# Performance work log

Hardware: AMD Instinct MI355X
Metric: run time of the kernel (lower is better)

Reference implementation:

```python
import jax, jax.numpy as jnp
import numpy as np

B, C, H, W = 8, 256, 128, 128
CQK = C // 8
EPS = 1e-6


def _l2n(x):
    # normalize over channel axis (dim=-2), matching torch l2_norm (no eps)
    return x / jnp.linalg.norm(x, axis=-2, keepdims=True)


def setup_inputs() -> dict:
    key = jax.random.key(0)
    ks = jax.random.split(key, 8)
    s = 0.05
    return {
        "x": jax.random.normal(ks[0], (B, C, H, W), dtype=jnp.float32),
        "Wq": jax.random.normal(ks[1], (CQK, C), dtype=jnp.float32) * s,
        "bq": jax.random.normal(ks[2], (CQK,), dtype=jnp.float32) * s,
        "Wk": jax.random.normal(ks[3], (CQK, C), dtype=jnp.float32) * s,
        "bk": jax.random.normal(ks[4], (CQK,), dtype=jnp.float32) * s,
        "Wv": jax.random.normal(ks[5], (C, C), dtype=jnp.float32) * s,
        "bv": jax.random.normal(ks[6], (C,), dtype=jnp.float32) * s,
        "gamma": jnp.ones((1,), dtype=jnp.float32) * 0.5,
    }


def reference(x, Wq, bq, Wk, bk, Wv, bv, gamma):
    b, c, h, w = x.shape
    n = h * w
    xf = x.reshape(b, c, n)  # [B, C, N]
    # 1x1 convs == channel matmuls
    Q = jnp.einsum('oc,bcn->bon', Wq, xf) + bq[None, :, None]  # [B, Cqk, N]
    K = jnp.einsum('oc,bcn->bon', Wk, xf) + bk[None, :, None]  # [B, Cqk, N]
    V = jnp.einsum('oc,bcn->bon', Wv, xf) + bv[None, :, None]  # [B, C, N]
    Qn = jnp.swapaxes(_l2n(Q), 1, 2)  # [B, N, Cqk]
    Kn = _l2n(K)                      # [B, Cqk, N]
    k_sum = jnp.sum(Kn, axis=-1) + EPS               # [B, Cqk]
    tailor = 1.0 / (n + jnp.einsum('bnc,bc->bn', Qn, k_sum))  # [B, N]
    value_sum = jnp.sum(V, axis=-1)                   # [B, C]
    matrix = jnp.einsum('bmn,bcn->bmc', Kn, V)        # [B, Cqk, C]
    matrix_sum = value_sum[:, :, None] + jnp.einsum('bnm,bmc->bcn', Qn, matrix)  # [B, C, N]
    weight_value = matrix_sum * tailor[:, None, :]    # [B, C, N]
    return x + gamma[0] * weight_value.reshape(b, c, h, w)
```

## Files before the change

### kernel.cpp

```cpp
#include <hip/hip_runtime.h>
#include <stdint.h>


#define NB 8
#define NC 256
#define CQK 32
#define NPIX 16384
#define NTILE 64
#define TN 256
#define PARTF (CQK*NC + NC + CQK)
#define EPSV 1e-6f

typedef unsigned short bfraw;

__device__ __forceinline__ float bf2f(bfraw u) {
    union { uint32_t i; float f; } v; v.i = ((uint32_t)u) << 16; return v.f;
}
__device__ __forceinline__ void unpack8(uint4 raw, float* xv) {
    xv[0] = bf2f((bfraw)(raw.x & 0xffffu)); xv[1] = bf2f((bfraw)(raw.x >> 16));
    xv[2] = bf2f((bfraw)(raw.y & 0xffffu)); xv[3] = bf2f((bfraw)(raw.y >> 16));
    xv[4] = bf2f((bfraw)(raw.z & 0xffffu)); xv[5] = bf2f((bfraw)(raw.z >> 16));
    xv[6] = bf2f((bfraw)(raw.w & 0xffffu)); xv[7] = bf2f((bfraw)(raw.w >> 16));
}
template<int DT> __device__ __forceinline__ float ldx(const void* p, size_t i) {
    if (DT) return ((const float*)p)[i];
    return bf2f(((const bfraw*)p)[i]);
}
template<int DT> __device__ __forceinline__ void ld8(const void* p, size_t i, float* o) {
    if (DT) {
        const float4* q = (const float4*)((const float*)p + i);
        float4 a = q[0], b = q[1];
        o[0]=a.x;o[1]=a.y;o[2]=a.z;o[3]=a.w;o[4]=b.x;o[5]=b.y;o[6]=b.z;o[7]=b.w;
    } else {
        uint4 raw = *(const uint4*)((const bfraw*)p + i);
        unpack8(raw, o);
    }
}

template<int DT> __device__ __forceinline__ void prep_body(
    const void* Wq, const void* bq, const void* Wk, const void* bk,
    float* wkqT, float* bkq) {
    int tid = threadIdx.x;
    for (int i = tid; i < CQK*NC; i += 256) {
        int m = i >> 8, c = i & 255;
        wkqT[c*64 + m]      = ldx<DT>(Wk, i);
        wkqT[c*64 + 32 + m] = ldx<DT>(Wq, i);
    }
    if (tid < CQK)      bkq[tid]      = ldx<DT>(bk, tid);
    else if (tid < 64)  bkq[tid]      = ldx<DT>(bq, tid - 32);
}
__global__ __launch_bounds__(256) void detprep_kernel(
    const bfraw* __restrict__ xr, const void* Wq, const void* bq,
    const void* Wk, const void* bk,
    int* __restrict__ flag, float* __restrict__ wkqT, float* __restrict__ bkq) {
    __shared__ int cnt, ez, fl_s;
    int tid = threadIdx.x;
    if (tid == 0) { cnt = 0; ez = 0; }
    __syncthreads();
    int crazy = 0, evenzero = 0;
    for (int i = tid; i < 2048; i += 256) {
        bfraw u = xr[i];
        float v = bf2f(u);
        float a = fabsf(v);
        if (!(a <= 1e10f) || (v != 0.f && a < 1e-10f)) crazy++;
        if ((i & 1) == 0 && u == 0) evenzero++;
    }
    atomicAdd(&cnt, crazy);
    atomicAdd(&ez, evenzero);
    __syncthreads();
    if (tid == 0) { fl_s = (cnt > 64 || ez > 900) ? 1 : 0; flag[0] = fl_s; }
    __syncthreads();
    if (fl_s) prep_body<1>(Wq, bq, Wk, bk, wkqT, bkq);
    else      prep_body<0>(Wq, bq, Wk, bk, wkqT, bkq);
}

template<int DT> __device__ __forceinline__ void pass1_body(
    const void* __restrict__ x, const float* __restrict__ wkqT,
    const float* __restrict__ bkq, float4* __restrict__ qn4,
    float* __restrict__ partial, int PB, float (*kn_s)[36]) {
    int tid = threadIdx.x;
    int b = blockIdx.x / PB, j = blockIdx.x % PB;

    float sacc[CQK];
    #pragma unroll
    for (int m = 0; m < CQK; ++m) sacc[m] = 0.f;
    float xsacc = 0.f, ksacc = 0.f;

    const size_t xb_base = (size_t)b * NC * NPIX;

    for (int tile = j; tile < NTILE; tile += PB) {
        int n0 = tile * TN;

        float kq[64];
        #pragma unroll
        for (int m = 0; m < 64; ++m) kq[m] = bkq[m];
        const size_t pixi = xb_base + n0 + tid;
        for (int c0 = 0; c0 < NC; c0 += 8) {
            float xv[8];
            #pragma unroll
            for (int jj = 0; jj < 8; ++jj)
                xv[jj] = ldx<DT>(x, pixi + (size_t)(c0+jj) * NPIX);
            #pragma unroll
            for (int jj = 0; jj < 8; ++jj) {
                const float4* w = (const float4*)(wkqT + (c0+jj)*64);
                #pragma unroll
                for (int m4 = 0; m4 < 16; ++m4) {
                    float4 wv = w[m4];
                    kq[m4*4+0] += wv.x * xv[jj]; kq[m4*4+1] += wv.y * xv[jj];
                    kq[m4*4+2] += wv.z * xv[jj]; kq[m4*4+3] += wv.w * xv[jj];
                }
            }
        }
        float ssk = 0.f, ssq = 0.f;
        #pragma unroll
        for (int m = 0; m < CQK; ++m) {
            ssk += kq[m]*kq[m]; ssq += kq[32+m]*kq[32+m];
        }
        float invk = rsqrtf(ssk), invq = rsqrtf(ssq);

        __syncthreads();
        #pragma unroll
        for (int m4 = 0; m4 < 8; ++m4) {
            float4 kv;
            kv.x = kq[m4*4+0]*invk; kv.y = kq[m4*4+1]*invk;
            kv.z = kq[m4*4+2]*invk; kv.w = kq[m4*4+3]*invk;
            *((float4*)&kn_s[tid][m4*4]) = kv;
        }
        __syncthreads();

        float4* qp = qn4 + (size_t)b * 8 * NPIX + (n0 + tid);
        #pragma unroll
        for (int m4 = 0; m4 < 8; ++m4) {
            float4 qv;
            qv.x = kq[32+m4*4+0]*invq; qv.y = kq[32+m4*4+1]*invq;
            qv.z = kq[32+m4*4+2]*invq; qv.w = kq[32+m4*4+3]*invq;
            qp[(size_t)m4 * NPIX] = qv;
        }

        const size_t rowbase = xb_base + (size_t)tid * NPIX + n0;
        for (int k0 = 0; k0 < TN; k0 += 8) {
            float xv[8]; ld8<DT>(x, rowbase + k0, xv);
            #pragma unroll
            for (int kk = 0; kk < 8; ++kk) {
                const float4* kr = (const float4*)&kn_s[k0+kk][0];
                float xvk = xv[kk];
                #pragma unroll
                for (int m4 = 0; m4 < 8; ++m4) {
                    float4 a = kr[m4];
                    sacc[m4*4+0] += a.x*xvk; sacc[m4*4+1] += a.y*xvk;
                    sacc[m4*4+2] += a.z*xvk; sacc[m4*4+3] += a.w*xvk;
                }
                xsacc += xvk;
            }
        }

        if (tid < CQK) {
            float s = 0.f;
            for (int t = 0; t < TN; ++t) s += kn_s[t][tid];
            ksacc += s;
        }
    }

    size_t base = (size_t)blockIdx.x * PARTF;
    #pragma unroll
    for (int m = 0; m < CQK; ++m) partial[base + m*NC + tid] = sacc[m];
    partial[base + CQK*NC + tid] = xsacc;
    if (tid < CQK) partial[base + CQK*NC + NC + tid] = ksacc;
}
__global__ __launch_bounds__(256) void pass1_kernel(
    const void* __restrict__ x, const float* __restrict__ wkqT,
    const float* __restrict__ bkq, float4* __restrict__ qn4,
    float* __restrict__ partial, int PB, const int* __restrict__ flag) {
    __shared__ __align__(16) float kn_s[TN][36];
    if (flag[0]) pass1_body<1>(x, wkqT, bkq, qn4, partial, PB, kn_s);
    else         pass1_body<0>(x, wkqT, bkq, qn4, partial, PB, kn_s);
}

template<int DT> __device__ __forceinline__ float dot256(const void* Wv, int row,
                                                         const float* sh) {
    float r = 0.f;
    for (int c0 = 0; c0 < NC; c0 += 8) {
        float xv[8]; ld8<DT>(Wv, (size_t)row * NC + c0, xv);
        #pragma unroll
        for (int i = 0; i < 8; ++i) r += xv[i] * sh[c0+i];
    }
    return r;
}
template<int DT> __device__ __forceinline__ void pass15_body(
    const float* __restrict__ partial, const void* __restrict__ Wv,
    const void* __restrict__ bv, float* __restrict__ matT,
    float* __restrict__ vsum, float* __restrict__ ksum, int PB, float* sh) {
    int tid = threadIdx.x;
    int b = blockIdx.x / 33, m = blockIdx.x % 33;
    const float* pb_ = partial + (size_t)b * PB * PARTF;

    if (m < CQK) {
        float acc = 0.f;
        for (int p = 0; p < PB; ++p) acc += pb_[(size_t)p*PARTF + m*NC + tid];
        sh[tid] = acc;
        float ks = 0.f;
        for (int p = 0; p < PB; ++p) ks += pb_[(size_t)p*PARTF + CQK*NC + NC + m];
        __syncthreads();
        float r = dot256<DT>(Wv, tid, sh);
        matT[((size_t)b*NC + tid)*CQK + m] = r + ldx<DT>(bv, tid) * ks;
        if (tid == 0) ksum[b*CQK + m] = ks + EPSV;
    } else {
        float acc = 0.f;
        for (int p = 0; p < PB; ++p) acc += pb_[(size_t)p*PARTF + CQK*NC + tid];
        sh[tid] = acc;
        __syncthreads();
        float r = dot256<DT>(Wv, tid, sh);
        vsum[b*NC + tid] = r + (float)NPIX * ldx<DT>(bv, tid);
    }
}
__global__ __launch_bounds__(256) void pass15_kernel(
    const float* __restrict__ partial, const void* __restrict__ Wv,
    const void* __restrict__ bv, float* __restrict__ matT,
    float* __restrict__ vsum, float* __restrict__ ksum, int PB,
    const int* __restrict__ flag) {
    __shared__ float sh[NC];
    if (flag[0]) pass15_body<1>(partial, Wv, bv, matT, vsum, ksum, PB, sh);
    else         pass15_body<0>(partial, Wv, bv, matT, vsum, ksum, PB, sh);
}

template<int DT> __device__ __forceinline__ void pass2_body(
    const void* __restrict__ x, const float4* __restrict__ qn4,
    const float* __restrict__ ksum, const float* __restrict__ matT,
    const float* __restrict__ vsum, const void* __restrict__ gamma,
    float* __restrict__ out) {
    int tid = threadIdx.x;
    int bx = blockIdx.x;
    int cs = bx & 3, tile = (bx >> 2) & 63, b = bx >> 8;
    int n0 = tile * TN;
    int p = n0 + tid;

    float q[CQK];
    const float4* qp = qn4 + (size_t)b * 8 * NPIX + p;
    #pragma unroll
    for (int m4 = 0; m4 < 8; ++m4) {
        float4 v = qp[(size_t)m4 * NPIX];
        q[m4*4+0]=v.x; q[m4*4+1]=v.y; q[m4*4+2]=v.z; q[m4*4+3]=v.w;
    }
    const float* ksb = ksum + b*CQK;
    float dot = 0.f;
    #pragma unroll
    for (int m = 0; m < CQK; ++m) dot += q[m] * ksb[m];
    float tl = 1.f / ((float)NPIX + dot);
    float gt = ldx<DT>(gamma, 0) * tl;

    int c0 = cs * 64;
    const float* mb = matT + ((size_t)b*NC + c0)*CQK;
    const float* vb = vsum + (size_t)b*NC + c0;
    size_t xbase = (size_t)b*NC*NPIX + (size_t)c0*NPIX + p;

    for (int ci = 0; ci < 64; ci += 4) {
        float xv[4];
        #pragma unroll
        for (int u = 0; u < 4; ++u)
            xv[u] = ldx<DT>(x, xbase + (size_t)(ci+u)*NPIX);
        #pragma unroll
        for (int u = 0; u < 4; ++u) {
            float r = vb[ci+u];
            const float4* mr = (const float4*)(mb + (ci+u)*CQK);
            #pragma unroll
            for (int m4 = 0; m4 < 8; ++m4) {
                float4 a = mr[m4];
                r += q[m4*4+0]*a.x + q[m4*4+1]*a.y + q[m4*4+2]*a.z + q[m4*4+3]*a.w;
            }
            out[xbase + (size_t)(ci+u)*NPIX] = xv[u] + gt*r;
        }
    }
}
__global__ __launch_bounds__(256) void pass2_kernel(
    const void* __restrict__ x, const float4* __restrict__ qn4,
    const float* __restrict__ ksum, const float* __restrict__ matT,
    const float* __restrict__ vsum, const void* __restrict__ gamma,
    float* __restrict__ out, const int* __restrict__ flag) {
    if (flag[0]) pass2_body<1>(x, qn4, ksum, matT, vsum, gamma, out);
    else         pass2_body<0>(x, qn4, ksum, matT, vsum, gamma, out);
}

extern "C" void kernel_launch(void* const* d_in, const int* in_sizes, int n_in,
                              void* d_out, int out_size, void* d_ws, size_t ws_size,
                              hipStream_t stream)
{
    const void* x  = d_in[0];
    const void* Wq = d_in[1];
    const void* bq = d_in[2];
    const void* Wk = d_in[3];
    const void* bk = d_in[4];
    const void* Wv = d_in[5];
    const void* bv = d_in[6];
    const void* gm = d_in[7];
    float* out = (float*)d_out;

    float* ws = (float*)d_ws;
    int*   flag = (int*)ws;
    float* wkqT = ws + 16;
    float* bkq  = wkqT + 64*NC;
    float* matT = bkq + 64;
    float* vsum = matT + NB*NC*CQK;
    float* ksum = vsum + NB*NC;
    float* qn4f = ksum + NB*CQK;
    float* partial = qn4f + (size_t)NB*8*NPIX*4;

    size_t fixedf = (size_t)(partial - ws);
    int PB = 64;
    while (PB > 1 && (fixedf + (size_t)NB*PB*PARTF) * 4 > ws_size) PB >>= 1;

    hipLaunchKernelGGL(detprep_kernel, dim3(1), dim3(256), 0, stream,
                       (const bfraw*)x, Wq, bq, Wk, bk, flag, wkqT, bkq);
    hipLaunchKernelGGL(pass1_kernel, dim3(NB*PB), dim3(256), 0, stream,
                       x, wkqT, bkq, (float4*)qn4f, partial, PB, flag);
    hipLaunchKernelGGL(pass15_kernel, dim3(NB*33), dim3(256), 0, stream,
                       partial, Wv, bv, matT, vsum, ksum, PB, flag);
    hipLaunchKernelGGL(pass2_kernel, dim3(NB*NTILE*4), dim3(256), 0, stream,
                       x, (const float4*)qn4f, ksum, matT, vsum, gm, out, flag);
}
```

Baseline: 489.6 us.

## Split pass1 channel projection across thread groups and process pixel pairs per thread

Pass1 now handles one 128-pixel tile per block across 128 blocks per batch. The 64 K/Q output channels are split into four 16-channel groups, each thread covers two adjacent pixels, and the L2 norms are reduced through shared memory. The k-sum reduction is parallelised over all threads instead of 32. Pass2 now processes two pixels per thread with float2 loads and stores, and both kernels get launch-bounds occupancy hints. The partial buffer falls back to the output buffer when the workspace is too small, which relies on pass2 overwriting it later.

```diff
diff --git a/kernel.cpp b/kernel.cpp
--- a/kernel.cpp
+++ b/kernel.cpp
@@ -6,8 +6,8 @@
 #define NC 256
 #define CQK 32
 #define NPIX 16384
-#define NTILE 64
-#define TN 256
+#define TN 128
+#define PB 128
 #define PARTF (CQK*NC + NC + CQK)
 #define EPSV 1e-6f
 
@@ -36,6 +36,15 @@
         unpack8(raw, o);
     }
 }
+template<int DT> __device__ __forceinline__ void ldx2(const void* p, size_t i, float* o) {
+    if (DT) {
+        float2 v = *(const float2*)((const float*)p + i);
+        o[0] = v.x; o[1] = v.y;
+    } else {
+        uint32_t r = *(const uint32_t*)((const bfraw*)p + i);
+        o[0] = bf2f((bfraw)(r & 0xffffu)); o[1] = bf2f((bfraw)(r >> 16));
+    }
+}
 
 template<int DT> __device__ __forceinline__ void prep_body(
     const void* Wq, const void* bq, const void* Wk, const void* bk,
@@ -77,103 +86,132 @@
 template<int DT> __device__ __forceinline__ void pass1_body(
     const void* __restrict__ x, const float* __restrict__ wkqT,
     const float* __restrict__ bkq, float4* __restrict__ qn4,
-    float* __restrict__ partial, int PB, float (*kn_s)[36]) {
-    int tid = threadIdx.x;
-    int b = blockIdx.x / PB, j = blockIdx.x % PB;
-
-    float sacc[CQK];
-    #pragma unroll
-    for (int m = 0; m < CQK; ++m) sacc[m] = 0.f;
-    float xsacc = 0.f, ksacc = 0.f;
-
-    const size_t xb_base = (size_t)b * NC * NPIX;
-
-    for (int tile = j; tile < NTILE; tile += PB) {
-        int n0 = tile * TN;
-
-        float kq[64];
-        #pragma unroll
-        for (int m = 0; m < 64; ++m) kq[m] = bkq[m];
-        const size_t pixi = xb_base + n0 + tid;
+    float* __restrict__ partial, float (*kn_s)[36], float* __restrict__ ss_s) {
+    const int tid  = threadIdx.x;
+    const int b    = blockIdx.x >> 7;
+    const int j    = blockIdx.x & (PB - 1);
+    const int n0   = j * TN;
+    const int pair = tid & 63;
+    const int g    = tid >> 6;
+    const size_t xb = (size_t)b * NC * NPIX;
+
+    float kq0[16], kq1[16];
+    #pragma unroll
+    for (int i = 0; i < 16; ++i) {
+        float bb = bkq[g*16 + i];
+        kq0[i] = bb; kq1[i] = bb;
+    }
+    {
+        const size_t pix0 = xb + (size_t)n0 + 2*pair;
         for (int c0 = 0; c0 < NC; c0 += 8) {
-            float xv[8];
+            float xv[8][2];
             #pragma unroll
             for (int jj = 0; jj < 8; ++jj)
-                xv[jj] = ldx<DT>(x, pixi + (size_t)(c0+jj) * NPIX);
+                ldx2<DT>(x, pix0 + (size_t)(c0 + jj) * NPIX, xv[jj]);
             #pragma unroll
             for (int jj = 0; jj < 8; ++jj) {
-                const float4* w = (const float4*)(wkqT + (c0+jj)*64);
+                const float4* w = (const float4*)(wkqT + (c0 + jj)*64 + g*16);
                 #pragma unroll
-                for (int m4 = 0; m4 < 16; ++m4) {
+                for (int m4 = 0; m4 < 4; ++m4) {
                     float4 wv = w[m4];
-                    kq[m4*4+0] += wv.x * xv[jj]; kq[m4*4+1] += wv.y * xv[jj];
-                    kq[m4*4+2] += wv.z * xv[jj]; kq[m4*4+3] += wv.w * xv[jj];
+                    kq0[m4*4+0] += wv.x * xv[jj][0]; kq0[m4*4+1] += wv.y * xv[jj][0];
+                    kq0[m4*4+2] += wv.z * xv[jj][0]; kq0[m4*4+3] += wv.w * xv[jj][0];
+                    kq1[m4*4+0] += wv.x * xv[jj][1]; kq1[m4*4+1] += wv.y * xv[jj][1];
+                    kq1[m4*4+2] += wv.z * xv[jj][1]; kq1[m4*4+3] += wv.w * xv[jj][1];
                 }
             }
         }
-        float ssk = 0.f, ssq = 0.f;
-        #pragma unroll
-        for (int m = 0; m < CQK; ++m) {
-            ssk += kq[m]*kq[m]; ssq += kq[32+m]*kq[32+m];
-        }
-        float invk = rsqrtf(ssk), invq = rsqrtf(ssq);
-
-        __syncthreads();
-        #pragma unroll
-        for (int m4 = 0; m4 < 8; ++m4) {
-            float4 kv;
-            kv.x = kq[m4*4+0]*invk; kv.y = kq[m4*4+1]*invk;
-            kv.z = kq[m4*4+2]*invk; kv.w = kq[m4*4+3]*invk;
-            *((float4*)&kn_s[tid][m4*4]) = kv;
-        }
-        __syncthreads();
-
-        float4* qp = qn4 + (size_t)b * 8 * NPIX + (n0 + tid);
-        #pragma unroll
-        for (int m4 = 0; m4 < 8; ++m4) {
-            float4 qv;
-            qv.x = kq[32+m4*4+0]*invq; qv.y = kq[32+m4*4+1]*invq;
-            qv.z = kq[32+m4*4+2]*invq; qv.w = kq[32+m4*4+3]*invq;
-            qp[(size_t)m4 * NPIX] = qv;
-        }
-
-        const size_t rowbase = xb_base + (size_t)tid * NPIX + n0;
-        for (int k0 = 0; k0 < TN; k0 += 8) {
-            float xv[8]; ld8<DT>(x, rowbase + k0, xv);
+    }
+
+    float ss0 = 0.f, ss1 = 0.f;
+    #pragma unroll
+    for (int i = 0; i < 16; ++i) { ss0 += kq0[i]*kq0[i]; ss1 += kq1[i]*kq1[i]; }
+    ss_s[(g*64 + pair)*2 + 0] = ss0;
+    ss_s[(g*64 + pair)*2 + 1] = ss1;
+    __syncthreads();
+
+    if (g < 2) {
+        float inv0 = rsqrtf(ss_s[(0*64+pair)*2+0] + ss_s[(1*64+pair)*2+0]);
+        float inv1 = rsqrtf(ss_s[(0*64+pair)*2+1] + ss_s[(1*64+pair)*2+1]);
+        float* r0 = &kn_s[2*pair  ][g*16];
+        float* r1 = &kn_s[2*pair+1][g*16];
+        #pragma unroll
+        for (int m4 = 0; m4 < 4; ++m4) {
+            float4 v0, v1;
+            v0.x = kq0[m4*4+0]*inv0; v0.y = kq0[m4*4+1]*inv0;
+            v0.z = kq0[m4*4+2]*inv0; v0.w = kq0[m4*4+3]*inv0;
+            v1.x = kq1[m4*4+0]*inv1; v1.y = kq1[m4*4+1]*inv1;
+            v1.z = kq1[m4*4+2]*inv1; v1.w = kq1[m4*4+3]*inv1;
+            *((float4*)&r0[m4*4]) = v0;
+            *((float4*)&r1[m4*4]) = v1;
+        }
+    } else {
+        float inv0 = rsqrtf(ss_s[(2*64+pair)*2+0] + ss_s[(3*64+pair)*2+0]);
+        float inv1 = rsqrtf(ss_s[(2*64+pair)*2+1] + ss_s[(3*64+pair)*2+1]);
+        float4* qp = qn4 + (size_t)b * 8 * NPIX + (n0 + 2*pair);
+        const int g2 = g - 2;
+        #pragma unroll
+        for (int m4 = 0; m4 < 4; ++m4) {
+            float4 v0, v1;
+            v0.x = kq0[m4*4+0]*inv0; v0.y = kq0[m4*4+1]*inv0;
+            v0.z = kq0[m4*4+2]*inv0; v0.w = kq0[m4*4+3]*inv0;
+            v1.x = kq1[m4*4+0]*inv1; v1.y = kq1[m4*4+1]*inv1;
+            v1.z = kq1[m4*4+2]*inv1; v1.w = kq1[m4*4+3]*inv1;
+            qp[(size_t)(g2*4 + m4) * NPIX]     = v0;
+            qp[(size_t)(g2*4 + m4) * NPIX + 1] = v1;
+        }
+    }
+    __syncthreads();
+
+    float sacc[CQK];
+    #pragma unroll
+    for (int m = 0; m < CQK; ++m) sacc[m] = 0.f;
+    float xsacc = 0.f;
+    const size_t rowb = xb + (size_t)tid * NPIX + n0;
+    for (int k0 = 0; k0 < TN; k0 += 8) {
+        float xv[8]; ld8<DT>(x, rowb + k0, xv);
+        #pragma unroll
+        for (int kk = 0; kk < 8; ++kk) {
+            const float4* kr = (const float4*)&kn_s[k0+kk][0];
+            float xvk = xv[kk];
             #pragma unroll
-            for (int kk = 0; kk < 8; ++kk) {
-                const float4* kr = (const float4*)&kn_s[k0+kk][0];
-                float xvk = xv[kk];
-                #pragma unroll
-                for (int m4 = 0; m4 < 8; ++m4) {
-                    float4 a = kr[m4];
-                    sacc[m4*4+0] += a.x*xvk; sacc[m4*4+1] += a.y*xvk;
-                    sacc[m4*4+2] += a.z*xvk; sacc[m4*4+3] += a.w*xvk;
-                }
-                xsacc += xvk;
+            for (int m4 = 0; m4 < 8; ++m4) {
+                float4 a = kr[m4];
+                sacc[m4*4+0] += a.x*xvk; sacc[m4*4+1] += a.y*xvk;
+                sacc[m4*4+2] += a.z*xvk; sacc[m4*4+3] += a.w*xvk;
             }
-        }
-
-        if (tid < CQK) {
-            float s = 0.f;
-            for (int t = 0; t < TN; ++t) s += kn_s[t][tid];
-            ksacc += s;
-        }
-    }
-
-    size_t base = (size_t)blockIdx.x * PARTF;
+            xsacc += xvk;
+        }
+    }
+
+    {
+        const int m_ = tid & 31, h_ = tid >> 5;
+        float kp = 0.f;
+        #pragma unroll
+        for (int t = 0; t < 16; ++t) kp += kn_s[h_*16 + t][m_];
+        ss_s[h_*32 + m_] = kp;
+    }
+    __syncthreads();
+
+    const size_t base = (size_t)blockIdx.x * PARTF;
     #pragma unroll
     for (int m = 0; m < CQK; ++m) partial[base + m*NC + tid] = sacc[m];
     partial[base + CQK*NC + tid] = xsacc;
-    if (tid < CQK) partial[base + CQK*NC + NC + tid] = ksacc;
-}
-__global__ __launch_bounds__(256) void pass1_kernel(
+    if (tid < CQK) {
+        float ks = 0.f;
+        #pragma unroll
+        for (int h = 0; h < 8; ++h) ks += ss_s[h*32 + tid];
+        partial[base + CQK*NC + NC + tid] = ks;
+    }
+}
+__global__ __launch_bounds__(256, 4) void pass1_kernel(
     const void* __restrict__ x, const float* __restrict__ wkqT,
     const float* __restrict__ bkq, float4* __restrict__ qn4,
-    float* __restrict__ partial, int PB, const int* __restrict__ flag) {
+    float* __restrict__ partial, const int* __restrict__ flag) {
     __shared__ __align__(16) float kn_s[TN][36];
-    if (flag[0]) pass1_body<1>(x, wkqT, bkq, qn4, partial, PB, kn_s);
-    else         pass1_body<0>(x, wkqT, bkq, qn4, partial, PB, kn_s);
+    __shared__ float ss_s[4*64*2];
+    if (flag[0]) pass1_body<1>(x, wkqT, bkq, qn4, partial, kn_s, ss_s);
+    else         pass1_body<0>(x, wkqT, bkq, qn4, partial, kn_s, ss_s);
 }
 
 template<int DT> __device__ __forceinline__ float dot256(const void* Wv, int row,
@@ -189,7 +227,7 @@
 template<int DT> __device__ __forceinline__ void pass15_body(
     const float* __restrict__ partial, const void* __restrict__ Wv,
     const void* __restrict__ bv, float* __restrict__ matT,
-    float* __restrict__ vsum, float* __restrict__ ksum, int PB, float* sh) {
+    float* __restrict__ vsum, float* __restrict__ ksum, float* sh) {
     int tid = threadIdx.x;
     int b = blockIdx.x / 33, m = blockIdx.x % 33;
     const float* pb_ = partial + (size_t)b * PB * PARTF;
@@ -216,11 +254,11 @@
 __global__ __launch_bounds__(256) void pass15_kernel(
     const float* __restrict__ partial, const void* __restrict__ Wv,
     const void* __restrict__ bv, float* __restrict__ matT,
-    float* __restrict__ vsum, float* __restrict__ ksum, int PB,
+    float* __restrict__ vsum, float* __restrict__ ksum,
     const int* __restrict__ flag) {
     __shared__ float sh[NC];
-    if (flag[0]) pass15_body<1>(partial, Wv, bv, matT, vsum, ksum, PB, sh);
-    else         pass15_body<0>(partial, Wv, bv, matT, vsum, ksum, PB, sh);
+    if (flag[0]) pass15_body<1>(partial, Wv, bv, matT, vsum, ksum, sh);
+    else         pass15_body<0>(partial, Wv, bv, matT, vsum, ksum, sh);
 }
 
 template<int DT> __device__ __forceinline__ void pass2_body(
@@ -230,48 +268,57 @@
     float* __restrict__ out) {
     int tid = threadIdx.x;
     int bx = blockIdx.x;
-    int cs = bx & 3, tile = (bx >> 2) & 63, b = bx >> 8;
-    int n0 = tile * TN;
-    int p = n0 + tid;
-
-    float q[CQK];
-    const float4* qp = qn4 + (size_t)b * 8 * NPIX + p;
+    int cs = bx & 3, tile = (bx >> 2) & 31, b = bx >> 7;
+    int p0 = tile * 512 + 2 * tid;
+
+    float q0[CQK], q1[CQK];
+    const float4* qp = qn4 + (size_t)b * 8 * NPIX + p0;
     #pragma unroll
     for (int m4 = 0; m4 < 8; ++m4) {
-        float4 v = qp[(size_t)m4 * NPIX];
-        q[m4*4+0]=v.x; q[m4*4+1]=v.y; q[m4*4+2]=v.z; q[m4*4+3]=v.w;
+        float4 a = qp[(size_t)m4 * NPIX];
+        float4 c = qp[(size_t)m4 * NPIX + 1];
+        q0[m4*4+0]=a.x; q0[m4*4+1]=a.y; q0[m4*4+2]=a.z; q0[m4*4+3]=a.w;
+        q1[m4*4+0]=c.x; q1[m4*4+1]=c.y; q1[m4*4+2]=c.z; q1[m4*4+3]=c.w;
     }
     const float* ksb = ksum + b*CQK;
-    float dot = 0.f;
-    #pragma unroll
-    for (int m = 0; m < CQK; ++m) dot += q[m] * ksb[m];
-    float tl = 1.f / ((float)NPIX + dot);
-    float gt = ldx<DT>(gamma, 0) * tl;
+    float dot0 = 0.f, dot1 = 0.f;
+    #pragma unroll
+    for (int m = 0; m < CQK; ++m) {
+        float k = ksb[m];
+        dot0 += q0[m] * k; dot1 += q1[m] * k;
+    }
+    float gm_ = ldx<DT>(gamma, 0);
+    float gt0 = gm_ / ((float)NPIX + dot0);
+    float gt1 = gm_ / ((float)NPIX + dot1);
 
     int c0 = cs * 64;
     const float* mb = matT + ((size_t)b*NC + c0)*CQK;
     const float* vb = vsum + (size_t)b*NC + c0;
-    size_t xbase = (size_t)b*NC*NPIX + (size_t)c0*NPIX + p;
+    size_t xbase = (size_t)b*NC*NPIX + (size_t)c0*NPIX + p0;
 
     for (int ci = 0; ci < 64; ci += 4) {
-        float xv[4];
+        float xv[4][2];
         #pragma unroll
         for (int u = 0; u < 4; ++u)
-            xv[u] = ldx<DT>(x, xbase + (size_t)(ci+u)*NPIX);
+            ldx2<DT>(x, xbase + (size_t)(ci+u)*NPIX, xv[u]);
         #pragma unroll
         for (int u = 0; u < 4; ++u) {
-            float r = vb[ci+u];
+            float r0 = vb[ci+u], r1 = r0;
             const float4* mr = (const float4*)(mb + (ci+u)*CQK);
             #pragma unroll
             for (int m4 = 0; m4 < 8; ++m4) {
                 float4 a = mr[m4];
-                r += q[m4*4+0]*a.x + q[m4*4+1]*a.y + q[m4*4+2]*a.z + q[m4*4+3]*a.w;
+                r0 += q0[m4*4+0]*a.x + q0[m4*4+1]*a.y + q0[m4*4+2]*a.z + q0[m4*4+3]*a.w;
+                r1 += q1[m4*4+0]*a.x + q1[m4*4+1]*a.y + q1[m4*4+2]*a.z + q1[m4*4+3]*a.w;
             }
-            out[xbase + (size_t)(ci+u)*NPIX] = xv[u] + gt*r;
-        }
-    }
-}
-__global__ __launch_bounds__(256) void pass2_kernel(
+            float2 o;
+            o.x = xv[u][0] + gt0*r0;
+            o.y = xv[u][1] + gt1*r1;
+            *reinterpret_cast<float2*>(out + xbase + (size_t)(ci+u)*NPIX) = o;
+        }
+    }
+}
+__global__ __launch_bounds__(256, 4) void pass2_kernel(
     const void* __restrict__ x, const float4* __restrict__ qn4,
     const float* __restrict__ ksum, const float* __restrict__ matT,
     const float* __restrict__ vsum, const void* __restrict__ gamma,
@@ -302,18 +349,18 @@
     float* vsum = matT + NB*NC*CQK;
     float* ksum = vsum + NB*NC;
     float* qn4f = ksum + NB*CQK;
-    float* partial = qn4f + (size_t)NB*8*NPIX*4;
-
-    size_t fixedf = (size_t)(partial - ws);
-    int PB = 64;
-    while (PB > 1 && (fixedf + (size_t)NB*PB*PARTF) * 4 > ws_size) PB >>= 1;
+    float* partial_ws = qn4f + (size_t)NB*8*NPIX*4;
+
+    size_t fixedf = (size_t)(partial_ws - ws);
+    size_t needb  = (fixedf + (size_t)NB*PB*PARTF) * sizeof(float);
+    float* partial = (needb <= ws_size) ? partial_ws : (float*)d_out;
 
     hipLaunchKernelGGL(detprep_kernel, dim3(1), dim3(256), 0, stream,
                        (const bfraw*)x, Wq, bq, Wk, bk, flag, wkqT, bkq);
     hipLaunchKernelGGL(pass1_kernel, dim3(NB*PB), dim3(256), 0, stream,
-                       x, wkqT, bkq, (float4*)qn4f, partial, PB, flag);
+                       x, wkqT, bkq, (float4*)qn4f, partial, flag);
     hipLaunchKernelGGL(pass15_kernel, dim3(NB*33), dim3(256), 0, stream,
-                       partial, Wv, bv, matT, vsum, ksum, PB, flag);
-    hipLaunchKernelGGL(pass2_kernel, dim3(NB*NTILE*4), dim3(256), 0, stream,
+                       partial, Wv, bv, matT, vsum, ksum, flag);
+    hipLaunchKernelGGL(pass2_kernel, dim3(NB*32*4), dim3(256), 0, stream,
                        x, (const float4*)qn4f, ksum, matT, vsum, gm, out, flag);
 }
```

Result: slower. 790.1 us (+61.4%).

## Split pass1 work across 512 threads with K/Q halves and pixel-half reduction

Applied to the files above, without the earlier changes.

Pass1 now runs 512 threads per block, with one tile per block. Each half of the threads computes either the K or the Q projection (32 outputs instead of 64), and the K^T·x accumulation is split across two pixel halves, then reduced through shared memory. This cuts per-thread register pressure and serial work in the projection, and raises parallelism per block. PB is fixed at 64, with a fallback that uses the output buffer as partial storage, and pass2 now loads 8 channels of x per iteration instead of 4. The cost is extra shared-memory exchange and barriers.

```diff
diff --git a/kernel.cpp b/kernel.cpp
--- a/kernel.cpp
+++ b/kernel.cpp
@@ -6,8 +6,8 @@
 #define NC 256
 #define CQK 32
 #define NPIX 16384
-#define NTILE 64
 #define TN 256
+#define PB1 64
 #define PARTF (CQK*NC + NC + CQK)
 #define EPSV 1e-6f
 
@@ -77,103 +77,122 @@
 template<int DT> __device__ __forceinline__ void pass1_body(
     const void* __restrict__ x, const float* __restrict__ wkqT,
     const float* __restrict__ bkq, float4* __restrict__ qn4,
-    float* __restrict__ partial, int PB, float (*kn_s)[36]) {
-    int tid = threadIdx.x;
-    int b = blockIdx.x / PB, j = blockIdx.x % PB;
-
-    float sacc[CQK];
-    #pragma unroll
-    for (int m = 0; m < CQK; ++m) sacc[m] = 0.f;
-    float xsacc = 0.f, ksacc = 0.f;
-
-    const size_t xb_base = (size_t)b * NC * NPIX;
-
-    for (int tile = j; tile < NTILE; tile += PB) {
-        int n0 = tile * TN;
-
-        float kq[64];
-        #pragma unroll
-        for (int m = 0; m < 64; ++m) kq[m] = bkq[m];
-        const size_t pixi = xb_base + n0 + tid;
-        for (int c0 = 0; c0 < NC; c0 += 8) {
-            float xv[8];
+    float* __restrict__ partial,
+    float (*kn_s)[36], float* __restrict__ ks2, float* __restrict__ xsx) {
+    const int tid  = threadIdx.x;
+    const int b    = blockIdx.x >> 6;
+    const int j    = blockIdx.x & (PB1 - 1);
+    const int n0   = j * TN;
+    const int px   = tid & 255;
+    const int half = tid >> 8;
+    const size_t xb = (size_t)b * NC * NPIX;
+
+    float kq[32];
+    #pragma unroll
+    for (int i = 0; i < 32; ++i) kq[i] = bkq[half*32 + i];
+    {
+        const size_t pixi = xb + (size_t)n0 + px;
+        for (int c = 0; c < NC; c += 2) {
+            float x0 = ldx<DT>(x, pixi + (size_t)c * NPIX);
+            float x1 = ldx<DT>(x, pixi + (size_t)(c+1) * NPIX);
+            const float4* w0 = (const float4*)(wkqT + c*64 + half*32);
+            const float4* w1 = (const float4*)(wkqT + (c+1)*64 + half*32);
             #pragma unroll
-            for (int jj = 0; jj < 8; ++jj)
-                xv[jj] = ldx<DT>(x, pixi + (size_t)(c0+jj) * NPIX);
-            #pragma unroll
-            for (int jj = 0; jj < 8; ++jj) {
-                const float4* w = (const float4*)(wkqT + (c0+jj)*64);
-                #pragma unroll
-                for (int m4 = 0; m4 < 16; ++m4) {
-                    float4 wv = w[m4];
-                    kq[m4*4+0] += wv.x * xv[jj]; kq[m4*4+1] += wv.y * xv[jj];
-                    kq[m4*4+2] += wv.z * xv[jj]; kq[m4*4+3] += wv.w * xv[jj];
-                }
+            for (int m4 = 0; m4 < 8; ++m4) {
+                float4 a = w0[m4], bb = w1[m4];
+                kq[m4*4+0] += a.x*x0; kq[m4*4+0] += bb.x*x1;
+                kq[m4*4+1] += a.y*x0; kq[m4*4+1] += bb.y*x1;
+                kq[m4*4+2] += a.z*x0; kq[m4*4+2] += bb.z*x1;
+                kq[m4*4+3] += a.w*x0; kq[m4*4+3] += bb.w*x1;
             }
         }
-        float ssk = 0.f, ssq = 0.f;
-        #pragma unroll
-        for (int m = 0; m < CQK; ++m) {
-            ssk += kq[m]*kq[m]; ssq += kq[32+m]*kq[32+m];
-        }
-        float invk = rsqrtf(ssk), invq = rsqrtf(ssq);
-
-        __syncthreads();
-        #pragma unroll
-        for (int m4 = 0; m4 < 8; ++m4) {
-            float4 kv;
-            kv.x = kq[m4*4+0]*invk; kv.y = kq[m4*4+1]*invk;
-            kv.z = kq[m4*4+2]*invk; kv.w = kq[m4*4+3]*invk;
-            *((float4*)&kn_s[tid][m4*4]) = kv;
-        }
-        __syncthreads();
-
-        float4* qp = qn4 + (size_t)b * 8 * NPIX + (n0 + tid);
-        #pragma unroll
-        for (int m4 = 0; m4 < 8; ++m4) {
-            float4 qv;
-            qv.x = kq[32+m4*4+0]*invq; qv.y = kq[32+m4*4+1]*invq;
-            qv.z = kq[32+m4*4+2]*invq; qv.w = kq[32+m4*4+3]*invq;
-            qp[(size_t)m4 * NPIX] = qv;
-        }
-
-        const size_t rowbase = xb_base + (size_t)tid * NPIX + n0;
-        for (int k0 = 0; k0 < TN; k0 += 8) {
-            float xv[8]; ld8<DT>(x, rowbase + k0, xv);
+    }
+    float ss = 0.f;
+    #pragma unroll
+    for (int i = 0; i < 32; ++i) ss += kq[i]*kq[i];
+    float inv = rsqrtf(ss);
+
+    if (half == 0) {
+        float4* r = (float4*)&kn_s[px][0];
+        #pragma unroll
+        for (int m4 = 0; m4 < 8; ++m4)
+            r[m4] = make_float4(kq[m4*4+0]*inv, kq[m4*4+1]*inv,
+                                kq[m4*4+2]*inv, kq[m4*4+3]*inv);
+    } else {
+        float4* qp = qn4 + (size_t)b * 8 * NPIX + (n0 + px);
+        #pragma unroll
+        for (int m4 = 0; m4 < 8; ++m4)
+            qp[(size_t)m4 * NPIX] =
+                make_float4(kq[m4*4+0]*inv, kq[m4*4+1]*inv,
+                            kq[m4*4+2]*inv, kq[m4*4+3]*inv);
+    }
+    __syncthreads();
+
+    float sacc[CQK];
+    #pragma unroll
+    for (int m = 0; m < CQK; ++m) sacc[m] = 0.f;
+    float xsacc = 0.f;
+    {
+        const int c = px, h = half;
+        const size_t rowb = xb + (size_t)c * NPIX + n0 + h * 128;
+        for (int k0 = 0; k0 < 128; k0 += 8) {
+            float xv[8]; ld8<DT>(x, rowb + k0, xv);
             #pragma unroll
             for (int kk = 0; kk < 8; ++kk) {
-                const float4* kr = (const float4*)&kn_s[k0+kk][0];
-                float xvk = xv[kk];
+                const float4* kr = (const float4*)&kn_s[h*128 + k0 + kk][0];
+                float xk = xv[kk];
                 #pragma unroll
                 for (int m4 = 0; m4 < 8; ++m4) {
                     float4 a = kr[m4];
-                    sacc[m4*4+0] += a.x*xvk; sacc[m4*4+1] += a.y*xvk;
-                    sacc[m4*4+2] += a.z*xvk; sacc[m4*4+3] += a.w*xvk;
+                    sacc[m4*4+0] += a.x*xk; sacc[m4*4+1] += a.y*xk;
+                    sacc[m4*4+2] += a.z*xk; sacc[m4*4+3] += a.w*xk;
                 }
-                xsacc += xvk;
+                xsacc += xk;
             }
         }
-
-        if (tid < CQK) {
-            float s = 0.f;
-            for (int t = 0; t < TN; ++t) s += kn_s[t][tid];
-            ksacc += s;
-        }
-    }
-
-    size_t base = (size_t)blockIdx.x * PARTF;
-    #pragma unroll
-    for (int m = 0; m < CQK; ++m) partial[base + m*NC + tid] = sacc[m];
-    partial[base + CQK*NC + tid] = xsacc;
-    if (tid < CQK) partial[base + CQK*NC + NC + tid] = ksacc;
-}
-__global__ __launch_bounds__(256) void pass1_kernel(
+    }
+
+    {
+        const int m_ = tid & 31, grp = tid >> 5;
+        float kp = 0.f;
+        #pragma unroll
+        for (int r = 0; r < 16; ++r) kp += kn_s[grp*16 + r][m_];
+        ks2[grp*32 + m_] = kp;
+    }
+    __syncthreads();
+
+    float* xch = (float*)kn_s;
+    if (half == 1) {
+        #pragma unroll
+        for (int m = 0; m < CQK; ++m) xch[m*NC + px] = sacc[m];
+        xsx[px] = xsacc;
+    }
+    __syncthreads();
+    const size_t base = (size_t)blockIdx.x * PARTF;
+    if (half == 0) {
+        #pragma unroll
+        for (int m = 0; m < CQK; ++m) sacc[m] += xch[m*NC + px];
+        xsacc += xsx[px];
+        #pragma unroll
+        for (int m = 0; m < CQK; ++m) partial[base + m*NC + px] = sacc[m];
+        partial[base + CQK*NC + px] = xsacc;
+    }
+    if (tid < CQK) {
+        float ks = 0.f;
+        #pragma unroll
+        for (int g = 0; g < 16; ++g) ks += ks2[g*32 + tid];
+        partial[base + CQK*NC + NC + tid] = ks;
+    }
+}
+__global__ __launch_bounds__(512) void pass1_kernel(
     const void* __restrict__ x, const float* __restrict__ wkqT,
     const float* __restrict__ bkq, float4* __restrict__ qn4,
-    float* __restrict__ partial, int PB, const int* __restrict__ flag) {
+    float* __restrict__ partial, const int* __restrict__ flag) {
     __shared__ __align__(16) float kn_s[TN][36];
-    if (flag[0]) pass1_body<1>(x, wkqT, bkq, qn4, partial, PB, kn_s);
-    else         pass1_body<0>(x, wkqT, bkq, qn4, partial, PB, kn_s);
+    __shared__ float ks2[16*32];
+    __shared__ float xsx[NC];
+    if (flag[0]) pass1_body<1>(x, wkqT, bkq, qn4, partial, kn_s, ks2, xsx);
+    else         pass1_body<0>(x, wkqT, bkq, qn4, partial, kn_s, ks2, xsx);
 }
 
 template<int DT> __device__ __forceinline__ float dot256(const void* Wv, int row,
@@ -189,24 +208,27 @@
 template<int DT> __device__ __forceinline__ void pass15_body(
     const float* __restrict__ partial, const void* __restrict__ Wv,
     const void* __restrict__ bv, float* __restrict__ matT,
-    float* __restrict__ vsum, float* __restrict__ ksum, int PB, float* sh) {
+    float* __restrict__ vsum, float* __restrict__ ksum, float* sh) {
     int tid = threadIdx.x;
     int b = blockIdx.x / 33, m = blockIdx.x % 33;
-    const float* pb_ = partial + (size_t)b * PB * PARTF;
+    const float* pb_ = partial + (size_t)b * PB1 * PARTF;
 
     if (m < CQK) {
         float acc = 0.f;
-        for (int p = 0; p < PB; ++p) acc += pb_[(size_t)p*PARTF + m*NC + tid];
+        #pragma unroll 4
+        for (int p = 0; p < PB1; ++p) acc += pb_[(size_t)p*PARTF + m*NC + tid];
         sh[tid] = acc;
         float ks = 0.f;
-        for (int p = 0; p < PB; ++p) ks += pb_[(size_t)p*PARTF + CQK*NC + NC + m];
+        #pragma unroll 4
+        for (int p = 0; p < PB1; ++p) ks += pb_[(size_t)p*PARTF + CQK*NC + NC + m];
         __syncthreads();
         float r = dot256<DT>(Wv, tid, sh);
         matT[((size_t)b*NC + tid)*CQK + m] = r + ldx<DT>(bv, tid) * ks;
         if (tid == 0) ksum[b*CQK + m] = ks + EPSV;
     } else {
         float acc = 0.f;
-        for (int p = 0; p < PB; ++p) acc += pb_[(size_t)p*PARTF + CQK*NC + tid];
+        #pragma unroll 4
+        for (int p = 0; p < PB1; ++p) acc += pb_[(size_t)p*PARTF + CQK*NC + tid];
         sh[tid] = acc;
         __syncthreads();
         float r = dot256<DT>(Wv, tid, sh);
@@ -216,11 +238,11 @@
 __global__ __launch_bounds__(256) void pass15_kernel(
     const float* __restrict__ partial, const void* __restrict__ Wv,
     const void* __restrict__ bv, float* __restrict__ matT,
-    float* __restrict__ vsum, float* __restrict__ ksum, int PB,
+    float* __restrict__ vsum, float* __restrict__ ksum,
     const int* __restrict__ flag) {
     __shared__ float sh[NC];
-    if (flag[0]) pass15_body<1>(partial, Wv, bv, matT, vsum, ksum, PB, sh);
-    else         pass15_body<0>(partial, Wv, bv, matT, vsum, ksum, PB, sh);
+    if (flag[0]) pass15_body<1>(partial, Wv, bv, matT, vsum, ksum, sh);
+    else         pass15_body<0>(partial, Wv, bv, matT, vsum, ksum, sh);
 }
 
 template<int DT> __device__ __forceinline__ void pass2_body(
@@ -231,35 +253,33 @@
     int tid = threadIdx.x;
     int bx = blockIdx.x;
     int cs = bx & 3, tile = (bx >> 2) & 63, b = bx >> 8;
-    int n0 = tile * TN;
-    int p = n0 + tid;
+    int p = tile * TN + tid;
 
     float q[CQK];
     const float4* qp = qn4 + (size_t)b * 8 * NPIX + p;
     #pragma unroll
     for (int m4 = 0; m4 < 8; ++m4) {
-        float4 v = qp[(size_t)m4 * NPIX];
-        q[m4*4+0]=v.x; q[m4*4+1]=v.y; q[m4*4+2]=v.z; q[m4*4+3]=v.w;
+        float4 a = qp[(size_t)m4 * NPIX];
+        q[m4*4+0]=a.x; q[m4*4+1]=a.y; q[m4*4+2]=a.z; q[m4*4+3]=a.w;
     }
     const float* ksb = ksum + b*CQK;
     float dot = 0.f;
     #pragma unroll
     for (int m = 0; m < CQK; ++m) dot += q[m] * ksb[m];
-    float tl = 1.f / ((float)NPIX + dot);
-    float gt = ldx<DT>(gamma, 0) * tl;
+    float gt = ldx<DT>(gamma, 0) / ((float)NPIX + dot);
 
     int c0 = cs * 64;
     const float* mb = matT + ((size_t)b*NC + c0)*CQK;
     const float* vb = vsum + (size_t)b*NC + c0;
     size_t xbase = (size_t)b*NC*NPIX + (size_t)c0*NPIX + p;
 
-    for (int ci = 0; ci < 64; ci += 4) {
-        float xv[4];
-        #pragma unroll
-        for (int u = 0; u < 4; ++u)
+    for (int ci = 0; ci < 64; ci += 8) {
+        float xv[8];
+        #pragma unroll
+        for (int u = 0; u < 8; ++u)
             xv[u] = ldx<DT>(x, xbase + (size_t)(ci+u)*NPIX);
         #pragma unroll
-        for (int u = 0; u < 4; ++u) {
+        for (int u = 0; u < 8; ++u) {
             float r = vb[ci+u];
             const float4* mr = (const float4*)(mb + (ci+u)*CQK);
             #pragma unroll
@@ -302,18 +322,18 @@
     float* vsum = matT + NB*NC*CQK;
     float* ksum = vsum + NB*NC;
     float* qn4f = ksum + NB*CQK;
-    float* partial = qn4f + (size_t)NB*8*NPIX*4;
-
-    size_t fixedf = (size_t)(partial - ws);
-    int PB = 64;
-    while (PB > 1 && (fixedf + (size_t)NB*PB*PARTF) * 4 > ws_size) PB >>= 1;
+    float* partial_ws = qn4f + (size_t)NB*8*NPIX*4;
+
+    size_t fixedf = (size_t)(partial_ws - ws);
+    size_t needb  = (fixedf + (size_t)NB*PB1*PARTF) * sizeof(float);
+    float* partial = (needb <= ws_size) ? partial_ws : (float*)d_out;
 
     hipLaunchKernelGGL(detprep_kernel, dim3(1), dim3(256), 0, stream,
                        (const bfraw*)x, Wq, bq, Wk, bk, flag, wkqT, bkq);
-    hipLaunchKernelGGL(pass1_kernel, dim3(NB*PB), dim3(256), 0, stream,
-                       x, wkqT, bkq, (float4*)qn4f, partial, PB, flag);
+    hipLaunchKernelGGL(pass1_kernel, dim3(NB*PB1), dim3(512), 0, stream,
+                       x, wkqT, bkq, (float4*)qn4f, partial, flag);
     hipLaunchKernelGGL(pass15_kernel, dim3(NB*33), dim3(256), 0, stream,
-                       partial, Wv, bv, matT, vsum, ksum, PB, flag);
-    hipLaunchKernelGGL(pass2_kernel, dim3(NB*NTILE*4), dim3(256), 0, stream,
+                       partial, Wv, bv, matT, vsum, ksum, flag);
+    hipLaunchKernelGGL(pass2_kernel, dim3(NB*64*4), dim3(256), 0, stream,
                        x, (const float4*)qn4f, ksum, matT, vsum, gm, out, flag);
 }
```

New measurement: 611.5 us. 1.25x slower.
